# Kernel optimization log

Hardware: AMD Instinct MI355X
Metric: run time of the kernel (lower is better)

The kernel has to match this reference:

```python
import jax, jax.numpy as jnp
import numpy as np

B, S, HID = 2, 1024, 4096
NH, NKV, HD = 32, 8, 128
SEL = 128      # outlier channels kept fp after reorder
GS = 128       # group size for weight / int4 KV quant
A_BITS, W_BITS, KV_BITS = 8, 4, 4
EPS = 1e-6
NEG = -1e30


def quantize_int_group(w, nbits, group_size):
    # asymmetric uint quant per group, dequantized back (pseudo-quant)
    shape = w.shape
    w2 = w.reshape(-1, group_size)
    q_max = 2 ** nbits - 1
    w_max = jnp.max(w2, axis=-1, keepdims=True)
    w_min = jnp.min(w2, axis=-1, keepdims=True)
    scales = jnp.maximum(w_max - w_min, 1e-5) / q_max
    base = jnp.clip(jnp.round(-w_min / scales), 0, q_max)
    wq = (jnp.clip(jnp.round(w2 / scales) + base, 0, q_max) - base) * scales
    return wq.reshape(shape)


def reorder_quantize_x(x, reorder_index, select_num, nbits):
    # reorder channels so outliers land at the end; int8 per-token quant of the rest
    x = x[:, reorder_index]
    x_low, x_keep = x[:, :-select_num], x[:, -select_num:]
    qmax = 2 ** (nbits - 1) - 1
    scale = jnp.maximum(jnp.max(jnp.abs(x_low), axis=-1, keepdims=True), 1e-5) / qmax
    x_q = jnp.clip(jnp.round(x_low / scale), -qmax - 1, qmax) * scale
    return x_q, x_keep


def qlinear(x_q, x_keep, W, reorder_index, select_num):
    # quantized part uses int4 group-quantized weights; outlier part stays fp
    Wr = W[:, reorder_index]
    W_low = quantize_int_group(Wr[:, :-select_num], W_BITS, GS)
    W_keep = Wr[:, -select_num:]
    return x_q @ W_low.T + x_keep @ W_keep.T


def rms_norm(x, w):
    var = jnp.mean(x * x, axis=-1, keepdims=True)
    return x * jax.lax.rsqrt(var + EPS) * w


def rotate_half(x):
    h = x.shape[-1] // 2
    return jnp.concatenate([-x[..., h:], x[..., :h]], axis=-1)


def setup_inputs() -> dict:
    key = jax.random.key(0)
    ks = jax.random.split(key, 8)
    hidden_states = jax.random.normal(ks[0], (B, S, HID), dtype=jnp.float32)
    # real RoPE tables (Qwen3 theta=1e6)
    inv_freq = 1.0 / (1e6 ** (np.arange(0, HD, 2, dtype=np.float32) / HD))
    t = np.arange(S, dtype=np.float32)
    freqs = np.outer(t, inv_freq)                  # [S, HD/2]
    emb = np.concatenate([freqs, freqs], axis=-1)  # [S, HD]
    cos = jnp.asarray(np.broadcast_to(np.cos(emb), (B, S, HD)).copy())
    sin = jnp.asarray(np.broadcast_to(np.sin(emb), (B, S, HD)).copy())
    sd = 0.02
    Wq = jax.random.normal(ks[1], (NH * HD, HID), dtype=jnp.float32) * sd
    Wk = jax.random.normal(ks[2], (NKV * HD, HID), dtype=jnp.float32) * sd
    Wv = jax.random.normal(ks[3], (NKV * HD, HID), dtype=jnp.float32) * sd
    Wo = jax.random.normal(ks[4], (HID, NH * HD), dtype=jnp.float32) * sd
    q_norm_w = jnp.ones((HD,), dtype=jnp.float32)
    k_norm_w = jnp.ones((HD,), dtype=jnp.float32)
    rng = np.random.default_rng(0)
    reorder_qkv = jnp.asarray(rng.permutation(HID).astype(np.int32))
    reorder_o = jnp.asarray(rng.permutation(NH * HD).astype(np.int32))
    return {"hidden_states": hidden_states, "cos": cos, "sin": sin,
            "Wq": Wq, "Wk": Wk, "Wv": Wv, "Wo": Wo,
            "q_norm_w": q_norm_w, "k_norm_w": k_norm_w,
            "reorder_qkv": reorder_qkv, "reorder_o": reorder_o}


def reference(hidden_states, cos, sin, Wq, Wk, Wv, Wo, q_norm_w, k_norm_w,
              reorder_qkv, reorder_o):
    x2 = hidden_states.reshape(B * S, HID)
    xq, xk = reorder_quantize_x(x2, reorder_qkv, SEL, A_BITS)
    q = qlinear(xq, xk, Wq, reorder_qkv, SEL).reshape(B, S, NH, HD)
    k = qlinear(xq, xk, Wk, reorder_qkv, SEL).reshape(B, S, NKV, HD)
    v = qlinear(xq, xk, Wv, reorder_qkv, SEL).reshape(B, S, NKV, HD).transpose(0, 2, 1, 3)
    q = rms_norm(q, q_norm_w).transpose(0, 2, 1, 3)   # [B,NH,S,HD]
    k = rms_norm(k, k_norm_w).transpose(0, 2, 1, 3)   # [B,NKV,S,HD]
    k = quantize_int_group(k, KV_BITS, GS)            # int4 KV-cache quant (pre-RoPE, as in source)
    c = cos[:, None, :, :]
    s = sin[:, None, :, :]
    q = q * c + rotate_half(q) * s
    k = k * c + rotate_half(k) * s
    rep = NH // NKV
    k = jnp.repeat(k, rep, axis=1)                    # repeat_kv
    v = jnp.repeat(v, rep, axis=1)
    v = quantize_int_group(v, KV_BITS, GS)            # int4 V quant (post repeat, as in source)
    scores = jnp.einsum('bhqd,bhkd->bhqk', q, k) / jnp.sqrt(jnp.float32(HD))
    mask = jnp.tril(jnp.ones((S, S), dtype=bool))     # is_causal=True path
    scores = jnp.where(mask, scores, NEG)
    attn = jax.nn.softmax(scores, axis=-1)
    out = jnp.einsum('bhqk,bhkd->bhqd', attn, v)
    out = out.transpose(0, 2, 1, 3).reshape(B * S, NH * HD)
    oq, ok = reorder_quantize_x(out, reorder_o, SEL, A_BITS)
    out = qlinear(oq, ok, Wo, reorder_o, SEL)
    return out.reshape(B, S, HID)
```

## Files before the change

kernel.cpp:

```cpp
#include <hip/hip_runtime.h>
#include <hip/hip_bf16.h>
#include <cstdint>

#define S_LEN 1024
#define HID   4096
#define NH    32
#define NKV   8
#define HD    128
#define NLOW  3968
#define M_ROWS 2048
#define NQKV  6144

typedef _Float16 f16_t;
typedef _Float16 f16x8 __attribute__((ext_vector_type(8)));
typedef float    f32x4 __attribute__((ext_vector_type(4)));

#define MFMA16(a,b,c) __builtin_amdgcn_mfma_f32_16x16x32_f16(a,b,c,0,0,0)

__device__ inline void gload16(const void* g, void* l) {
  __builtin_amdgcn_global_load_lds(
      (const __attribute__((address_space(1))) void*)g,
      (__attribute__((address_space(3))) void*)l, 16, 0, 0);
}

#define WAITV(n) asm volatile("s_waitcnt vmcnt(" #n ")" ::: "memory")
#define LGKM0()  asm volatile("s_waitcnt lgkmcnt(0)" ::: "memory")
#define FENCE()  asm volatile("" ::: "memory")

__device__ inline float wred_max(float v){ for(int o=32;o;o>>=1) v=fmaxf(v,__shfl_xor(v,o)); return v; }
__device__ inline float wred_min(float v){ for(int o=32;o;o>>=1) v=fminf(v,__shfl_xor(v,o)); return v; }
__device__ inline float wred_sum(float v){ for(int o=32;o;o>>=1) v+=__shfl_xor(v,o); return v; }

__global__ __launch_bounds__(256) void aquant_kernel(const float* __restrict__ X,
                                                     const int* __restrict__ reorder,
                                                     f16_t* __restrict__ out,
                                                     float* __restrict__ sarr)
{
  __shared__ float xs[HID];
  __shared__ float red[256];
  int row = blockIdx.x;
  int t = threadIdx.x;
  const float* xr = X + (size_t)row * HID;
  float amax = 0.f;
  for (int c = t; c < HID; c += 256) {
    float v = xr[reorder[c]];
    xs[c] = v;
    if (c < NLOW) amax = fmaxf(amax, fabsf(v));
  }
  red[t] = amax;
  __syncthreads();
  for (int s = 128; s > 0; s >>= 1) {
    if (t < s) red[t] = fmaxf(red[t], red[t + s]);
    __syncthreads();
  }
  float scale = fmaxf(red[0], 1e-5f) / 127.0f;
  if (t == 0) sarr[row] = scale;
  f16_t* orow = out + (size_t)row * HID;
  for (int c = t; c < HID; c += 256) {
    float v = xs[c];
    if (c < NLOW) {
      float q = fminf(fmaxf(rintf(v / scale), -128.f), 127.f);
      orow[c] = (f16_t)q;
    } else {
      orow[c] = (f16_t)(v / scale);
    }
  }
}

__device__ inline void wquant_body(const float* __restrict__ wrowbase,
                                   const int* __restrict__ reorder,
                                   f16_t* __restrict__ orow, int t, float* xs)
{
  const f32x4* wrow4 = (const f32x4*)wrowbase;
  f32x4* xs4 = (f32x4*)xs;
  #pragma unroll
  for (int i = 0; i < 4; i++)
    xs4[t + i * 256] = wrow4[t + i * 256];
  __syncthreads();

  int c0 = t * 16;
  float v[16];
  #pragma unroll
  for (int j = 0; j < 16; j++)
    v[j] = xs[reorder[c0 + j]];

  f16x8 o0, o1;
  if (c0 < NLOW) {
    float mn = v[0], mx = v[0];
    #pragma unroll
    for (int j = 1; j < 16; j++) { mn = fminf(mn, v[j]); mx = fmaxf(mx, v[j]); }
    #pragma unroll
    for (int o = 1; o <= 4; o <<= 1) {
      mn = fminf(mn, __shfl_xor(mn, o));
      mx = fmaxf(mx, __shfl_xor(mx, o));
    }
    float scale = fmaxf(mx - mn, 1e-5f) / 15.0f;
    float base = fminf(fmaxf(rintf(-mn / scale), 0.f), 15.f);
    #pragma unroll
    for (int j = 0; j < 8; j++) {
      o0[j] = (f16_t)((fminf(fmaxf(rintf(v[j] / scale) + base, 0.f), 15.f) - base) * scale);
      o1[j] = (f16_t)((fminf(fmaxf(rintf(v[j + 8] / scale) + base, 0.f), 15.f) - base) * scale);
    }
  } else {
    #pragma unroll
    for (int j = 0; j < 8; j++) { o0[j] = (f16_t)v[j]; o1[j] = (f16_t)v[j + 8]; }
  }
  *(f16x8*)(orow + c0) = o0;
  *(f16x8*)(orow + c0 + 8) = o1;
}

__global__ __launch_bounds__(256) void wquant_kernel(const float* __restrict__ W,
                                                     const int* __restrict__ reorder,
                                                     f16_t* __restrict__ out)
{
  __shared__ float xs[HID];
  int row = blockIdx.x;
  wquant_body(W + (size_t)row * HID, reorder, out + (size_t)row * HID, threadIdx.x, xs);
}

__global__ __launch_bounds__(256) void wquant3_kernel(const float* __restrict__ Wq,
                                                      const float* __restrict__ Wk,
                                                      const float* __restrict__ Wv,
                                                      const int* __restrict__ reorder,
                                                      f16_t* __restrict__ out)
{
  __shared__ float xs[HID];
  int row = blockIdx.x;
  const float* src = (row < 4096) ? Wq + (size_t)row * HID
                   : (row < 5120) ? Wk + (size_t)(row - 4096) * HID
                                  : Wv + (size_t)(row - 5120) * HID;
  wquant_body(src, reorder, out + (size_t)row * HID, threadIdx.x, xs);
}

template<int BM_, int BN_, int WM, typename OT>
__global__ __launch_bounds__(512, 4) void gemm_bt(const f16_t* __restrict__ A,
                                                  const f16_t* __restrict__ Bm,
                                                  OT* __restrict__ C,
                                                  const float* __restrict__ rowscale,
                                                  int N, int K)
{
  constexpr int WN   = 8 / WM;
  constexpr int MREP = BM_ / WM / 16;
  constexpr int NREP = BN_ / WN / 16;
  constexpr int ACH  = BM_ / 8;
  constexpr int TCH  = ACH + BN_ / 8;
  constexpr int CPW  = TCH / 8;
  static_assert(TCH % 8 == 0, "chunks must split evenly across 8 waves");
  __shared__ f16_t As[2][BM_ * 64];
  __shared__ f16_t Bs[2][BN_ * 64];

  int tid = threadIdx.x;
  int w = tid >> 6, lane = tid & 63;
  int g = lane >> 4, l15 = lane & 15;
  int wm = w / WN, wn = w % WN;
  int gm0 = blockIdx.y * BM_, gn0 = blockIdx.x * BN_;
  int NT = K >> 6;
  int srow = lane >> 3;
  int sslot = (lane & 7) ^ srow;

  f32x4 acc[MREP][NREP];
  #pragma unroll
  for (int m = 0; m < MREP; m++)
    #pragma unroll
    for (int n = 0; n < NREP; n++) acc[m][n] = f32x4{0.f, 0.f, 0.f, 0.f};

  auto STAGE = [&](int t, int s) {
    #pragma unroll
    for (int i = 0; i < CPW; i++) {
      int ch = w + 8 * i;
      if (ch < ACH) {
        int r = ch * 8 + srow;
        gload16(A + (size_t)(gm0 + r) * K + t * 64 + sslot * 8, &As[s][ch * 512]);
      } else {
        int cb = ch - ACH;
        int r = cb * 8 + srow;
        gload16(Bm + (size_t)(gn0 + r) * K + t * 64 + sslot * 8, &Bs[s][cb * 512]);
      }
    }
  };

  STAGE(0, 0);
  for (int t = 0; t < NT; t++) {
    int cur = t & 1;
    if (t + 1 < NT) {
      STAGE(t + 1, cur ^ 1);
      if constexpr (CPW == 7)      { WAITV(7); }
      else if constexpr (CPW == 6) { WAITV(6); }
      else if constexpr (CPW == 5) { WAITV(5); }
      else                         { WAITV(4); }
    } else {
      WAITV(0);
    }
    FENCE();
    __builtin_amdgcn_s_barrier();
    FENCE();

    f16x8 afr[MREP][2];
    #pragma unroll
    for (int m = 0; m < MREP; m++) {
      int r = wm * (BM_ / WM) + m * 16 + l15;
      #pragma unroll
      for (int kk = 0; kk < 2; kk++)
        afr[m][kk] = *(const f16x8*)(&As[cur][r * 64 + (((kk * 4 + g) ^ (r & 7)) * 8)]);
    }
    __builtin_amdgcn_s_setprio(1);
    #pragma unroll
    for (int n = 0; n < NREP; n++) {
      int r = wn * (BN_ / WN) + n * 16 + l15;
      f16x8 b0 = *(const f16x8*)(&Bs[cur][r * 64 + ((g ^ (r & 7)) * 8)]);
      f16x8 b1 = *(const f16x8*)(&Bs[cur][r * 64 + (((4 + g) ^ (r & 7)) * 8)]);
      #pragma unroll
      for (int m = 0; m < MREP; m++) {
        acc[m][n] = MFMA16(afr[m][0], b0, acc[m][n]);
        acc[m][n] = MFMA16(afr[m][1], b1, acc[m][n]);
      }
    }
    __builtin_amdgcn_s_setprio(0);
    LGKM0();
    __builtin_amdgcn_s_barrier();
    FENCE();
  }

  #pragma unroll
  for (int m = 0; m < MREP; m++)
    #pragma unroll
    for (int j = 0; j < 4; j++) {
      int grow = gm0 + wm * (BM_ / WM) + m * 16 + g * 4 + j;
      float sc = rowscale[grow];
      #pragma unroll
      for (int n = 0; n < NREP; n++) {
        int gcol = gn0 + wn * (BN_ / WN) + n * 16 + l15;
        C[(size_t)grow * N + gcol] = (OT)(acc[m][n][j] * sc);
      }
    }
}

__global__ __launch_bounds__(512) void post_kernel(const f16_t* __restrict__ qkv,
                                                   const float* __restrict__ cosb,
                                                   const float* __restrict__ sinb,
                                                   const float* __restrict__ qnw,
                                                   const float* __restrict__ knw,
                                                   f16_t* __restrict__ Q,
                                                   f16_t* __restrict__ K)
{
  int m = blockIdx.x;
  int b = m >> 10, s = m & 1023;
  int tid = threadIdx.x;
  int w = tid >> 6, l = tid & 63;

  float c0 = cosb[(size_t)m * HD + l];
  float c1 = cosb[(size_t)m * HD + 64 + l];
  float s0 = sinb[(size_t)m * HD + l];
  float s1 = sinb[(size_t)m * HD + 64 + l];
  float qw0 = qnw[l], qw1 = qnw[64 + l];
  float kw0 = knw[l], kw1 = knw[64 + l];
  const f16_t* row = qkv + (size_t)m * NQKV;

  #pragma unroll
  for (int it = 0; it < 5; it++) {
    int slot = it * 8 + w;
    const f16_t* hp = row + slot * HD;
    float x0 = (float)hp[l];
    float x1 = (float)hp[l + 64];
    if (slot < NH) {
      int h = slot;
      float ss = wred_sum(x0 * x0 + x1 * x1);
      float r = 1.0f / sqrtf(ss * (1.0f / 128.0f) + 1e-6f);
      float xn0 = x0 * r * qw0, xn1 = x1 * r * qw1;
      float o0 = (xn0 * c0 - xn1 * s0) * 0.08838834764831845f;
      float o1 = (xn1 * c1 + xn0 * s1) * 0.08838834764831845f;
      f16_t* qp = Q + (((size_t)(b * NH + h)) * S_LEN + s) * HD;
      qp[l] = (f16_t)o0;
      qp[l + 64] = (f16_t)o1;
    } else {
      int h = slot - NH;
      float ss = wred_sum(x0 * x0 + x1 * x1);
      float r = 1.0f / sqrtf(ss * (1.0f / 128.0f) + 1e-6f);
      float xn0 = x0 * r * kw0, xn1 = x1 * r * kw1;
      float mn = wred_min(fminf(xn0, xn1));
      float mx = wred_max(fmaxf(xn0, xn1));
      float scale = fmaxf(mx - mn, 1e-5f) / 15.0f;
      float base = fminf(fmaxf(rintf(-mn / scale), 0.f), 15.f);
      float q0 = (fminf(fmaxf(rintf(xn0 / scale) + base, 0.f), 15.f) - base) * scale;
      float q1 = (fminf(fmaxf(rintf(xn1 / scale) + base, 0.f), 15.f) - base) * scale;
      float o0 = q0 * c0 - q1 * s0;
      float o1 = q1 * c1 + q0 * s1;
      f16_t* kp = K + (((size_t)(b * NKV + h)) * S_LEN + s) * HD;
      kp[l] = (f16_t)o0;
      kp[l + 64] = (f16_t)o1;
    }
  }
}

__global__ __launch_bounds__(256) void vtrans_kernel(const f16_t* __restrict__ qkv,
                                                     f16_t* __restrict__ Vt)
{
  __shared__ f16_t vs[128][129];
  int blk = blockIdx.x;
  int st = blk & 7;
  int bh = blk >> 3;
  int b = bh >> 3, h = bh & 7;
  int s0 = st * 128;
  int t = threadIdx.x;

  int r = t >> 1, hf = t & 1;
  const f16_t* src = qkv + ((size_t)(b * S_LEN + s0 + r)) * NQKV + (NH + NKV + h) * HD + hf * 64;
  #pragma unroll
  for (int i = 0; i < 8; i++)
    *(f16x8*)(&vs[r][hf * 64 + i * 8]) = *(const f16x8*)(src + i * 8);
  __syncthreads();

  float mn = 1e30f, mx = -1e30f;
  #pragma unroll
  for (int i = 0; i < 64; i++) {
    float x = (float)vs[r][hf * 64 + i];
    mn = fminf(mn, x); mx = fmaxf(mx, x);
  }
  mn = fminf(mn, __shfl_xor(mn, 1));
  mx = fmaxf(mx, __shfl_xor(mx, 1));
  float scale = fmaxf(mx - mn, 1e-5f) / 15.0f;
  float base = fminf(fmaxf(rintf(-mn / scale), 0.f), 15.f);
  #pragma unroll
  for (int i = 0; i < 64; i++) {
    int d = hf * 64 + i;
    float x = (float)vs[r][d];
    vs[r][d] = (f16_t)((fminf(fmaxf(rintf(x / scale) + base, 0.f), 15.f) - base) * scale);
  }
  __syncthreads();

  int wv = t >> 6, ln = t & 63;
  #pragma unroll
  for (int dd = 0; dd < 32; dd++) {
    int d = wv * 32 + dd;
    f16_t* orow = Vt + ((size_t)bh * HD + d) * S_LEN + s0;
    orow[ln] = vs[ln][d];
    orow[64 + ln] = vs[64 + ln][d];
  }
}

__global__ __launch_bounds__(512) void attn_mfma(const f16_t* __restrict__ Q,
                                                 const f16_t* __restrict__ Kg,
                                                 const f16_t* __restrict__ Vg,
                                                 float* __restrict__ O)
{
  __shared__ f16_t Ks[2][64 * 128];
  __shared__ f16_t Vs[2][128 * 64];
  __shared__ f16_t Ps[8 * 16 * 64];
  int tid = threadIdx.x;
  int w = tid >> 6, lane = tid & 63;
  int g = lane >> 4, l15 = lane & 15;
  int flat = blockIdx.x;
  int h = flat & 31, b = (flat >> 5) & 1, qb = flat >> 6;
  int kvh = h >> 2;
  int q0 = qb * 128;

  const f16_t* Qp = Q + (size_t)(b * NH + h) * S_LEN * HD;
  const f16_t* Kp = Kg + (size_t)(b * NKV + kvh) * S_LEN * HD;
  const f16_t* Vp = Vg + (size_t)(b * NKV + kvh) * HD * S_LEN;

  int qrow = q0 + w * 16 + l15;
  int myqmax = q0 + w * 16 + 15;
  f16x8 qf[4];
  #pragma unroll
  for (int c = 0; c < 4; c++)
    qf[c] = *(const f16x8*)(Qp + (size_t)qrow * HD + c * 32 + g * 8);

  f32x4 zf = {0.f, 0.f, 0.f, 0.f};
  f32x4 oacc[8];
  #pragma unroll
  for (int nd = 0; nd < 8; nd++) oacc[nd] = zf;
  float mrun[4], lrun[4];
  #pragma unroll
  for (int j = 0; j < 4; j++) { mrun[j] = -INFINITY; lrun[j] = 0.f; }

  int vrow = lane >> 3, vslot = lane & 7;
  auto STAGEKV = [&](int it, int bb) {
    int kt = it * 64;
    #pragma unroll
    for (int i = 0; i < 2; i++) {
      int c = w + 8 * i;
      int row = c * 4 + g;
      gload16(Kp + (size_t)(kt + row) * HD + (l15 ^ (row & 7)) * 8, &Ks[bb][c * 512]);
    }
    #pragma unroll
    for (int i = 0; i < 2; i++) {
      int c = w + 8 * i;
      int row = c * 8 + vrow;
      gload16(Vp + (size_t)row * S_LEN + kt + (vslot ^ (row & 7)) * 8, &Vs[bb][c * 512]);
    }
  };

  f16_t* pw = Ps + w * 1024;
  int ntiles = 2 * qb + 2;
  STAGEKV(0, 0);
  for (int it = 0; it < ntiles; it++) {
    int cur = it & 1;
    if (it + 1 < ntiles) {
      STAGEKV(it + 1, cur ^ 1);
      WAITV(4);
    } else {
      WAITV(0);
    }
    FENCE();
    __builtin_amdgcn_s_barrier();
    FENCE();

    int kt = it * 64;
    if (kt <= myqmax) {
      f32x4 sv[4];
      #pragma unroll
      for (int nk = 0; nk < 4; nk++) sv[nk] = zf;
      __builtin_amdgcn_s_setprio(1);
      #pragma unroll
      for (int nk = 0; nk < 4; nk++) {
        int krow = nk * 16 + l15;
        #pragma unroll
        for (int c = 0; c < 4; c++) {
          f16x8 kf = *(const f16x8*)(&Ks[cur][krow * 128 + (((c * 4 + g) ^ (krow & 7)) * 8)]);
          sv[nk] = MFMA16(qf[c], kf, sv[nk]);
        }
      }
      __builtin_amdgcn_s_setprio(0);
      #pragma unroll
      for (int nk = 0; nk < 4; nk++) {
        int kcol = kt + nk * 16 + l15;
        #pragma unroll
        for (int j = 0; j < 4; j++) {
          int qr = q0 + w * 16 + g * 4 + j;
          if (kcol > qr) sv[nk][j] = -1e30f;
        }
      }
      float alpha[4];
      #pragma unroll
      for (int j = 0; j < 4; j++) {
        float mr = fmaxf(fmaxf(sv[0][j], sv[1][j]), fmaxf(sv[2][j], sv[3][j]));
        mr = fmaxf(mr, __shfl_xor(mr, 1));
        mr = fmaxf(mr, __shfl_xor(mr, 2));
        mr = fmaxf(mr, __shfl_xor(mr, 4));
        mr = fmaxf(mr, __shfl_xor(mr, 8));
        float mnew = fmaxf(mrun[j], mr);
        alpha[j] = __expf(mrun[j] - mnew);
        float lt = 0.f;
        #pragma unroll
        for (int nk = 0; nk < 4; nk++) {
          float p = __expf(sv[nk][j] - mnew);
          sv[nk][j] = p;
          lt += p;
        }
        lt += __shfl_xor(lt, 1);
        lt += __shfl_xor(lt, 2);
        lt += __shfl_xor(lt, 4);
        lt += __shfl_xor(lt, 8);
        lrun[j] = lrun[j] * alpha[j] + lt;
        mrun[j] = mnew;
      }
      #pragma unroll
      for (int j = 0; j < 4; j++) {
        int ql = g * 4 + j;
        #pragma unroll
        for (int nk = 0; nk < 4; nk++) {
          int kl = nk * 16 + l15;
          int ss = (kl >> 3) ^ (ql & 7);
          pw[ql * 64 + ss * 8 + (kl & 7)] = (f16_t)sv[nk][j];
        }
      }
      #pragma unroll
      for (int nd = 0; nd < 8; nd++)
        #pragma unroll
        for (int j = 0; j < 4; j++) oacc[nd][j] *= alpha[j];
      __builtin_amdgcn_s_setprio(1);
      #pragma unroll
      for (int kc = 0; kc < 2; kc++) {
        f16x8 pf = *(const f16x8*)(pw + l15 * 64 + ((kc * 4 + g) ^ (l15 & 7)) * 8);
        #pragma unroll
        for (int nd = 0; nd < 8; nd++) {
          int d = nd * 16 + l15;
          f16x8 vf = *(const f16x8*)(&Vs[cur][d * 64 + (((kc * 4 + g) ^ (d & 7)) * 8)]);
          oacc[nd] = MFMA16(pf, vf, oacc[nd]);
        }
      }
      __builtin_amdgcn_s_setprio(0);
      LGKM0();
    }
    __builtin_amdgcn_s_barrier();
    FENCE();
  }
  #pragma unroll
  for (int j = 0; j < 4; j++) {
    float invl = 1.0f / lrun[j];
    float* orow = O + ((size_t)(b * S_LEN) + q0 + w * 16 + g * 4 + j) * (NH * HD) + h * HD + l15;
    #pragma unroll
    for (int nd = 0; nd < 8; nd++) orow[nd * 16] = oacc[nd][j] * invl;
  }
}

extern "C" void kernel_launch(void* const* d_in, const int* in_sizes, int n_in,
                              void* d_out, int out_size, void* d_ws, size_t ws_size,
                              hipStream_t stream) {
  const float* hidden = (const float*)d_in[0];
  const float* cosb   = (const float*)d_in[1];
  const float* sinb   = (const float*)d_in[2];
  const float* Wq     = (const float*)d_in[3];
  const float* Wk     = (const float*)d_in[4];
  const float* Wv     = (const float*)d_in[5];
  const float* Wo     = (const float*)d_in[6];
  const float* qnw    = (const float*)d_in[7];
  const float* knw    = (const float*)d_in[8];
  const int*   r_qkv  = (const int*)d_in[9];
  const int*   r_o    = (const int*)d_in[10];
  float* out = (float*)d_out;

  f16_t* xq   = (f16_t*)d_ws;
  f16_t* wcat = xq + (size_t)M_ROWS * HID;
  f16_t* qkv  = wcat + (size_t)NQKV * HID;
  f16_t* Qb   = qkv + (size_t)M_ROWS * NQKV;
  f16_t* Kb   = Qb + (size_t)2 * NH * S_LEN * HD;
  f16_t* Vt   = Kb + (size_t)2 * NKV * S_LEN * HD;
  float* sa1  = (float*)(Vt + (size_t)2 * NKV * S_LEN * HD);
  float* sa2  = sa1 + M_ROWS;
  float* ao   = sa2 + M_ROWS;
  size_t needed = (size_t)((char*)(ao + (size_t)M_ROWS * HID) - (char*)d_ws);
  if (ws_size < needed) return;
  f16_t* oq  = xq;
  f16_t* woq = wcat;

  aquant_kernel<<<M_ROWS, 256, 0, stream>>>(hidden, r_qkv, xq, sa1);
  wquant3_kernel<<<NQKV, 256, 0, stream>>>(Wq, Wk, Wv, r_qkv, wcat);
  gemm_bt<128, 192, 2, f16_t><<<dim3(NQKV / 192, M_ROWS / 128), 512, 0, stream>>>(xq, wcat, qkv, sa1, NQKV, HID);
  post_kernel<<<M_ROWS, 512, 0, stream>>>(qkv, cosb, sinb, qnw, knw, Qb, Kb);
  vtrans_kernel<<<2 * NKV * 8, 256, 0, stream>>>(qkv, Vt);
  attn_mfma<<<512, 512, 0, stream>>>(Qb, Kb, Vt, ao);
  aquant_kernel<<<M_ROWS, 256, 0, stream>>>(ao, r_o, oq, sa2);
  wquant_kernel<<<4096, 256, 0, stream>>>(Wo, r_o, woq);
  gemm_bt<128, 128, 2, float><<<dim3(HID / 128, M_ROWS / 128), 512, 0, stream>>>(oq, woq, out, sa2, HID, HID);
}
```

Measured before the change: 362.9 us.

## Vectorize activation quant, merge all weight quant into one launch, balance causal attention

The activation quant kernel now loads each row coalesced into shared memory, gathers 16 reordered values per thread, reduces the max with wave shuffles instead of a tree of barriers, and writes 16-byte vector stores. The QKV and O weight quantization are merged into a single launch writing to a separate workspace buffer, which removes one kernel launch and gives more blocks per launch. The attention block index mapping pairs short and long causal query blocks so early-dispatched blocks mix light and heavy work. The workspace grows by one HID×HID f16 buffer.

```diff
diff --git a/kernel.cpp b/kernel.cpp
--- a/kernel.cpp
+++ b/kernel.cpp
@@ -37,34 +37,47 @@
                                                      float* __restrict__ sarr)
 {
   __shared__ float xs[HID];
-  __shared__ float red[256];
+  __shared__ float red[4];
   int row = blockIdx.x;
   int t = threadIdx.x;
-  const float* xr = X + (size_t)row * HID;
+  const f32x4* xr4 = (const f32x4*)(X + (size_t)row * HID);
+  f32x4* xs4 = (f32x4*)xs;
+  #pragma unroll
+  for (int i = 0; i < 4; i++)
+    xs4[t + i * 256] = xr4[t + i * 256];
+  __syncthreads();
+
+  int c0 = t * 16;
+  float v[16];
+  #pragma unroll
+  for (int j = 0; j < 16; j++)
+    v[j] = xs[reorder[c0 + j]];
+
   float amax = 0.f;
-  for (int c = t; c < HID; c += 256) {
-    float v = xr[reorder[c]];
-    xs[c] = v;
-    if (c < NLOW) amax = fmaxf(amax, fabsf(v));
-  }
-  red[t] = amax;
+  if (c0 < NLOW) {
+    #pragma unroll
+    for (int j = 0; j < 16; j++) amax = fmaxf(amax, fabsf(v[j]));
+  }
+  amax = wred_max(amax);
+  if ((t & 63) == 0) red[t >> 6] = amax;
   __syncthreads();
-  for (int s = 128; s > 0; s >>= 1) {
-    if (t < s) red[t] = fmaxf(red[t], red[t + s]);
-    __syncthreads();
-  }
-  float scale = fmaxf(red[0], 1e-5f) / 127.0f;
+  float scale = fmaxf(fmaxf(fmaxf(red[0], red[1]), fmaxf(red[2], red[3])), 1e-5f) / 127.0f;
   if (t == 0) sarr[row] = scale;
+
   f16_t* orow = out + (size_t)row * HID;
-  for (int c = t; c < HID; c += 256) {
-    float v = xs[c];
-    if (c < NLOW) {
-      float q = fminf(fmaxf(rintf(v / scale), -128.f), 127.f);
-      orow[c] = (f16_t)q;
-    } else {
-      orow[c] = (f16_t)(v / scale);
-    }
-  }
+  f16x8 o0, o1;
+  if (c0 < NLOW) {
+    #pragma unroll
+    for (int j = 0; j < 8; j++) {
+      o0[j] = (f16_t)fminf(fmaxf(rintf(v[j] / scale), -128.f), 127.f);
+      o1[j] = (f16_t)fminf(fmaxf(rintf(v[j + 8] / scale), -128.f), 127.f);
+    }
+  } else {
+    #pragma unroll
+    for (int j = 0; j < 8; j++) { o0[j] = (f16_t)(v[j] / scale); o1[j] = (f16_t)(v[j + 8] / scale); }
+  }
+  *(f16x8*)(orow + c0) = o0;
+  *(f16x8*)(orow + c0 + 8) = o1;
 }
 
 __device__ inline void wquant_body(const float* __restrict__ wrowbase,
@@ -109,27 +122,23 @@
   *(f16x8*)(orow + c0 + 8) = o1;
 }
 
-__global__ __launch_bounds__(256) void wquant_kernel(const float* __restrict__ W,
-                                                     const int* __restrict__ reorder,
-                                                     f16_t* __restrict__ out)
+__global__ __launch_bounds__(256) void wquant_all(const float* __restrict__ Wq,
+                                                  const float* __restrict__ Wk,
+                                                  const float* __restrict__ Wv,
+                                                  const float* __restrict__ Wo,
+                                                  const int* __restrict__ r_qkv,
+                                                  const int* __restrict__ r_o,
+                                                  f16_t* __restrict__ wcat,
+                                                  f16_t* __restrict__ woq)
 {
   __shared__ float xs[HID];
   int row = blockIdx.x;
-  wquant_body(W + (size_t)row * HID, reorder, out + (size_t)row * HID, threadIdx.x, xs);
-}
-
-__global__ __launch_bounds__(256) void wquant3_kernel(const float* __restrict__ Wq,
-                                                      const float* __restrict__ Wk,
-                                                      const float* __restrict__ Wv,
-                                                      const int* __restrict__ reorder,
-                                                      f16_t* __restrict__ out)
-{
-  __shared__ float xs[HID];
-  int row = blockIdx.x;
-  const float* src = (row < 4096) ? Wq + (size_t)row * HID
-                   : (row < 5120) ? Wk + (size_t)(row - 4096) * HID
-                                  : Wv + (size_t)(row - 5120) * HID;
-  wquant_body(src, reorder, out + (size_t)row * HID, threadIdx.x, xs);
+  const float* src; const int* reo; f16_t* dst;
+  if (row < 4096)      { src = Wq + (size_t)row * HID;          reo = r_qkv; dst = wcat + (size_t)row * HID; }
+  else if (row < 5120) { src = Wk + (size_t)(row - 4096) * HID; reo = r_qkv; dst = wcat + (size_t)row * HID; }
+  else if (row < 6144) { src = Wv + (size_t)(row - 5120) * HID; reo = r_qkv; dst = wcat + (size_t)row * HID; }
+  else                 { src = Wo + (size_t)(row - 6144) * HID; reo = r_o;   dst = woq + (size_t)(row - 6144) * HID; }
+  wquant_body(src, reo, dst, threadIdx.x, xs);
 }
 
 template<int BM_, int BN_, int WM, typename OT>
@@ -349,8 +358,12 @@
   int tid = threadIdx.x;
   int w = tid >> 6, lane = tid & 63;
   int g = lane >> 4, l15 = lane & 15;
-  int flat = blockIdx.x;
-  int h = flat & 31, b = (flat >> 5) & 1, qb = flat >> 6;
+  int i = blockIdx.x;
+  int base = i & 255, half = i >> 8;
+  int bh = base & 63;
+  int b = bh >> 5, h = bh & 31;
+  int qbase = base >> 6;
+  int qb = half ? 7 - qbase : qbase;
   int kvh = h >> 2;
   int q0 = qb * 128;
 
@@ -377,14 +390,14 @@
   auto STAGEKV = [&](int it, int bb) {
     int kt = it * 64;
     #pragma unroll
-    for (int i = 0; i < 2; i++) {
-      int c = w + 8 * i;
+    for (int ii = 0; ii < 2; ii++) {
+      int c = w + 8 * ii;
       int row = c * 4 + g;
       gload16(Kp + (size_t)(kt + row) * HD + (l15 ^ (row & 7)) * 8, &Ks[bb][c * 512]);
     }
     #pragma unroll
-    for (int i = 0; i < 2; i++) {
-      int c = w + 8 * i;
+    for (int ii = 0; ii < 2; ii++) {
+      int c = w + 8 * ii;
       int row = c * 8 + vrow;
       gload16(Vp + (size_t)row * S_LEN + kt + (vslot ^ (row & 7)) * 8, &Vs[bb][c * 512]);
     }
@@ -512,7 +525,8 @@
 
   f16_t* xq   = (f16_t*)d_ws;
   f16_t* wcat = xq + (size_t)M_ROWS * HID;
-  f16_t* qkv  = wcat + (size_t)NQKV * HID;
+  f16_t* woq  = wcat + (size_t)NQKV * HID;
+  f16_t* qkv  = woq + (size_t)HID * HID;
   f16_t* Qb   = qkv + (size_t)M_ROWS * NQKV;
   f16_t* Kb   = Qb + (size_t)2 * NH * S_LEN * HD;
   f16_t* Vt   = Kb + (size_t)2 * NKV * S_LEN * HD;
@@ -521,16 +535,14 @@
   float* ao   = sa2 + M_ROWS;
   size_t needed = (size_t)((char*)(ao + (size_t)M_ROWS * HID) - (char*)d_ws);
   if (ws_size < needed) return;
-  f16_t* oq  = xq;
-  f16_t* woq = wcat;
+  f16_t* oq = xq;
 
   aquant_kernel<<<M_ROWS, 256, 0, stream>>>(hidden, r_qkv, xq, sa1);
-  wquant3_kernel<<<NQKV, 256, 0, stream>>>(Wq, Wk, Wv, r_qkv, wcat);
+  wquant_all<<<NQKV + HID, 256, 0, stream>>>(Wq, Wk, Wv, Wo, r_qkv, r_o, wcat, woq);
   gemm_bt<128, 192, 2, f16_t><<<dim3(NQKV / 192, M_ROWS / 128), 512, 0, stream>>>(xq, wcat, qkv, sa1, NQKV, HID);
   post_kernel<<<M_ROWS, 512, 0, stream>>>(qkv, cosb, sinb, qnw, knw, Qb, Kb);
   vtrans_kernel<<<2 * NKV * 8, 256, 0, stream>>>(qkv, Vt);
   attn_mfma<<<512, 512, 0, stream>>>(Qb, Kb, Vt, ao);
   aquant_kernel<<<M_ROWS, 256, 0, stream>>>(ao, r_o, oq, sa2);
-  wquant_kernel<<<4096, 256, 0, stream>>>(Wo, r_o, woq);
   gemm_bt<128, 128, 2, float><<<dim3(HID / 128, M_ROWS / 128), 512, 0, stream>>>(oq, woq, out, sa2, HID, HID);
 }
```

Result: faster. 300.0 us (-17.3%).
